# Optimization experiments

Hardware: AMD Instinct MI355X
Metric: run time of the kernel (lower is better)

Reference implementation:

```python
import jax, jax.numpy as jnp
import numpy as np

DIM_IN = 1024
DIM_OUT = 1024
NUM_HEADS = 16
HEAD_DIM = DIM_OUT // NUM_HEADS


def setup_inputs() -> dict:
    key = jax.random.key(0)
    k1, k2, k3, k4 = jax.random.split(key, 4)
    X = jax.random.normal(k1, (4, 2048, DIM_IN), dtype=jnp.float32)
    W_qkv = jax.random.normal(k2, (DIM_IN, 3 * DIM_OUT), dtype=jnp.float32) * (DIM_IN ** -0.5)
    W_out = jax.random.normal(k3, (DIM_OUT, DIM_OUT), dtype=jnp.float32) * (DIM_OUT ** -0.5)
    b_out = jax.random.normal(k4, (DIM_OUT,), dtype=jnp.float32) * 0.01
    return {"X": X, "W_qkv": W_qkv, "W_out": W_out, "b_out": b_out}


def reference(X, W_qkv, W_out, b_out):
    B, S, _ = X.shape
    qkv = X @ W_qkv  # [B, S, 3*dim_out]
    qkv = qkv.reshape(B, S, 3, NUM_HEADS, HEAD_DIM).transpose(2, 0, 3, 1, 4)
    q, k, v = qkv[0], qkv[1], qkv[2]  # each [B, H, S, hd]
    scores = jnp.einsum('bhqd,bhkd->bhqk', q, k)  # [B, H, S, S]
    causal = jnp.triu(jnp.ones((S, S), dtype=bool), k=1)
    scores = jnp.where(causal, -jnp.inf, scores)
    attn = jax.nn.softmax(scores * (HEAD_DIM ** -0.5), axis=-1)
    ctx = jnp.einsum('bhqk,bhkd->bhqd', attn, v)  # [B, H, S, hd]
    ctx = ctx.transpose(0, 2, 1, 3).reshape(B, S, DIM_OUT)
    return ctx @ W_out + b_out
```

## Files before the change

kernel.cpp:

```cpp
#include <hip/hip_runtime.h>
#include <hip/hip_bf16.h>

typedef __bf16 bf16_t;
typedef __bf16 bf16x8 __attribute__((ext_vector_type(8)));
typedef __bf16 bf16x4 __attribute__((ext_vector_type(4)));
typedef float f32x4 __attribute__((ext_vector_type(4)));
typedef float f32x16 __attribute__((ext_vector_type(16)));
typedef unsigned int u32x4 __attribute__((ext_vector_type(4)));

#define AS1(p) ((const __attribute__((address_space(1))) void*)(p))
#define AS3(p) ((__attribute__((address_space(3))) void*)(p))

#define QSCALE 0.1803368801111204f

__global__ void cast_x_kernel(const float* __restrict__ X, bf16_t* __restrict__ Xb) {
  int i = (blockIdx.x * 256 + threadIdx.x) * 4;
  float4 v = *(const float4*)(X + i);
  bf16x4 o;
  o[0] = (bf16_t)v.x; o[1] = (bf16_t)v.y; o[2] = (bf16_t)v.z; o[3] = (bf16_t)v.w;
  *(bf16x4*)(Xb + i) = o;
}

__global__ void transpose_cast_kernel(const float* __restrict__ W, bf16_t* __restrict__ Wt,
                                      int K, int N) {
  __shared__ float tile[32][33];
  int n0 = blockIdx.x * 32, k0 = blockIdx.y * 32;
  int tx = threadIdx.x, ty = threadIdx.y;
  for (int r = ty; r < 32; r += 8)
    tile[r][tx] = W[(size_t)(k0 + r) * N + n0 + tx];
  __syncthreads();
  for (int r = ty; r < 32; r += 8)
    Wt[(size_t)(n0 + r) * K + k0 + tx] = (bf16_t)tile[tx][r];
}

__global__ __launch_bounds__(256) void gemm_qkv_kernel(
    const bf16_t* __restrict__ A, const bf16_t* __restrict__ Bt,
    bf16_t* __restrict__ Qb, bf16_t* __restrict__ Kb, bf16_t* __restrict__ Vt) {
  __shared__ __align__(16) bf16_t As[128 * 32];
  __shared__ __align__(16) bf16_t Bs[128 * 32];
  const int tid = threadIdx.x;
  const int lane = tid & 63, wave = tid >> 6;
  const int quad = lane >> 4, l15 = lane & 15;
  const int wr = wave >> 1, wc = wave & 1;
  const int m0 = blockIdx.x * 128, n0 = blockIdx.y * 128;
  f32x4 acc[4][4];
  const f32x4 vzero = {0.f, 0.f, 0.f, 0.f};
#pragma unroll
  for (int i = 0; i < 4; i++)
#pragma unroll
    for (int j = 0; j < 4; j++) acc[i][j] = vzero;

  for (int kb = 0; kb < 1024; kb += 32) {
    __syncthreads();
#pragma unroll
    for (int i = 0; i < 2; i++) {
      int c = i * 256 + tid;
      int row = c >> 2, kc = c & 3;
      __builtin_amdgcn_global_load_lds(AS1(A + (size_t)(m0 + row) * 1024 + kb + kc * 8),
                                       AS3(As + c * 8), 16, 0, 0);
    }
#pragma unroll
    for (int i = 0; i < 2; i++) {
      int c = i * 256 + tid;
      int row = c >> 2, kc = c & 3;
      __builtin_amdgcn_global_load_lds(AS1(Bt + (size_t)(n0 + row) * 1024 + kb + kc * 8),
                                       AS3(Bs + c * 8), 16, 0, 0);
    }
    __builtin_amdgcn_s_waitcnt(0);
    __syncthreads();
    bf16x8 af[4], bfr[4];
#pragma unroll
    for (int t = 0; t < 4; t++) {
      af[t]  = *(const bf16x8*)(As + (wr * 64 + t * 16 + l15) * 32 + quad * 8);
      bfr[t] = *(const bf16x8*)(Bs + (wc * 64 + t * 16 + l15) * 32 + quad * 8);
    }
#pragma unroll
    for (int mt = 0; mt < 4; mt++)
#pragma unroll
      for (int nt = 0; nt < 4; nt++)
        acc[mt][nt] = __builtin_amdgcn_mfma_f32_16x16x32_bf16(af[mt], bfr[nt], acc[mt][nt], 0, 0, 0);
  }
#pragma unroll
  for (int nt = 0; nt < 4; nt++) {
    int gn = n0 + wc * 64 + nt * 16 + l15;
    int which = gn >> 10;
    int rem = gn & 1023;
    int hh = rem >> 6, dd = rem & 63;
    if (which == 2) {
#pragma unroll
      for (int mt = 0; mt < 4; mt++) {
        int gm0 = m0 + wr * 64 + mt * 16 + quad * 4;
        int b = gm0 >> 11, s = gm0 & 2047;
        bf16x4 o;
#pragma unroll
        for (int r = 0; r < 4; r++) o[r] = (bf16_t)acc[mt][nt][r];
        *(bf16x4*)(Vt + ((size_t)((b << 4) + hh) * 64 + dd) * 2048 + s) = o;
      }
    } else {
      bf16_t* dst = (which == 0) ? Qb : Kb;
      float scl = (which == 0) ? QSCALE : 1.0f;
#pragma unroll
      for (int mt = 0; mt < 4; mt++) {
#pragma unroll
        for (int r = 0; r < 4; r++) {
          int gm = m0 + wr * 64 + mt * 16 + quad * 4 + r;
          int b = gm >> 11, s = gm & 2047;
          dst[((size_t)((b << 4) + hh) * 2048 + s) * 64 + dd] = (bf16_t)(acc[mt][nt][r] * scl);
        }
      }
    }
  }
}

__device__ inline unsigned pack_bf16x2(float a, float b) {
  unsigned short lo = __builtin_bit_cast(unsigned short, (bf16_t)a);
  unsigned short hi = __builtin_bit_cast(unsigned short, (bf16_t)b);
  return (unsigned)lo | ((unsigned)hi << 16);
}

__global__ __launch_bounds__(256, 4) void attn_kernel(
    const bf16_t* __restrict__ Qg_, const bf16_t* __restrict__ Kg_,
    const bf16_t* __restrict__ Vtg_, bf16_t* __restrict__ ctx) {
  __shared__ __align__(16) bf16_t Ksm[2][64 * 64];
  __shared__ __align__(16) bf16_t Vsm[2][64 * 64];
  const int tid = threadIdx.x;
  const int lane = tid & 63, w = tid >> 6;
  const int l31 = lane & 31, hl = lane >> 5;
  const int krow = (l31 & 0x13) | ((l31 & 4) << 1) | ((l31 & 8) >> 1);

  const int bh = blockIdx.x & 63;
  const int g = blockIdx.x >> 6;
  const int gr = g >> 2, gc = g & 3;
  const int qb = (gr == 0) ? (15 - gc) : (gr == 1) ? (8 + gc) : (gr == 2) ? (7 - gc) : gc;
  const int b = bh >> 4, h = bh & 15;
  const size_t base = (size_t)bh * 2048 * 64;
  const bf16_t* Qg = Qg_ + base;
  const bf16_t* Kg = Kg_ + base;
  const bf16_t* Vtg = Vtg_ + base;

  int kadr[4];
#pragma unroll
  for (int kk = 0; kk < 4; kk++)
    kadr[kk] = (krow * 8 + ((kk * 2 + hl) ^ (krow & 7))) * 8;
  int vadr[2];
#pragma unroll
  for (int nv = 0; nv < 2; nv++) {
    const int dr = nv * 32 + l31;
    vadr[nv] = (dr * 8 + (hl ^ (dr & 7))) * 8;
  }

  auto stage_kv = [&](int bb, int jn) {
#pragma unroll
    for (int i = 0; i < 2; i++) {
      int slot = i * 256 + tid;
      int row = slot >> 3, c = (slot & 7) ^ (row & 7);
      __builtin_amdgcn_global_load_lds(AS1(Kg + ((size_t)jn * 64 + row) * 64 + c * 8),
                                       AS3(&Ksm[bb][0] + slot * 8), 16, 0, 0);
    }
#pragma unroll
    for (int i = 0; i < 2; i++) {
      int slot = i * 256 + tid;
      int d = slot >> 3, c = (slot & 7) ^ (d & 7);
      __builtin_amdgcn_global_load_lds(AS1(Vtg + (size_t)d * 2048 + jn * 64 + c * 8),
                                       AS3(&Vsm[bb][0] + slot * 8), 16, 0, 0);
    }
  };

  bf16x8 bone;
#pragma unroll
  for (int e = 0; e < 8; e++) bone[e] = (bf16_t)1.0f;
  f32x16 zc;
#pragma unroll
  for (int e = 0; e < 16; e++) zc[e] = 0.f;

  const int J = 2 * (qb + 1);
  const int qrel = qb * 128 + w * 32;
  const int qg = qrel + l31;

  bf16x8 aq[4];
#pragma unroll
  for (int kk = 0; kk < 4; kk++)
    aq[kk] = *(const bf16x8*)(Qg + (size_t)qg * 64 + kk * 16 + hl * 8);

  f32x16 Oacc[2], Lacc;
#pragma unroll
  for (int e = 0; e < 16; e++) { Oacc[0][e] = 0.f; Oacc[1][e] = 0.f; Lacc[e] = 0.f; }

  int cur = 0;
  stage_kv(0, 0);

  for (int j = 0; j < J; j++) {
    asm volatile("s_waitcnt vmcnt(0)" ::: "memory");
    __syncthreads();
    if (j + 1 < J) stage_kv(cur ^ 1, j + 1);

    const bf16_t* Kb = &Ksm[cur][0];
    const bf16_t* Vb = &Vsm[cur][0];
    const int k0 = j * 64;

    auto nt_body = [&](int nt, bool masked) {
      __builtin_amdgcn_s_setprio(1);
      bf16x8 ak = *(const bf16x8*)(Kb + nt * 2048 + kadr[0]);
      f32x16 sc = __builtin_amdgcn_mfma_f32_32x32x16_bf16(ak, aq[0], zc, 0, 0, 0);
#pragma unroll
      for (int kk = 1; kk < 4; kk++) {
        ak = *(const bf16x8*)(Kb + nt * 2048 + kadr[kk]);
        sc = __builtin_amdgcn_mfma_f32_32x32x16_bf16(ak, aq[kk], sc, 0, 0, 0);
      }
      __builtin_amdgcn_s_setprio(0);

      float p[16];
#pragma unroll
      for (int r = 0; r < 16; r++) {
        const int koff = hl * 8 + (r & 7) + 16 * (r >> 3);
        p[r] = (masked && (koff > l31)) ? 0.f : __builtin_exp2f(sc[r]);
      }

      u32x4 w0, w1;
      w0[0] = pack_bf16x2(p[0], p[1]);   w0[1] = pack_bf16x2(p[2], p[3]);
      w0[2] = pack_bf16x2(p[4], p[5]);   w0[3] = pack_bf16x2(p[6], p[7]);
      w1[0] = pack_bf16x2(p[8], p[9]);   w1[1] = pack_bf16x2(p[10], p[11]);
      w1[2] = pack_bf16x2(p[12], p[13]); w1[3] = pack_bf16x2(p[14], p[15]);
      bf16x8 pa0 = __builtin_bit_cast(bf16x8, w0);
      bf16x8 pa1 = __builtin_bit_cast(bf16x8, w1);

      __builtin_amdgcn_s_setprio(1);
      Lacc = __builtin_amdgcn_mfma_f32_32x32x16_bf16(pa0, bone, Lacc, 0, 0, 0);
      Lacc = __builtin_amdgcn_mfma_f32_32x32x16_bf16(pa1, bone, Lacc, 0, 0, 0);
#pragma unroll
      for (int nv = 0; nv < 2; nv++) {
        bf16x8 bv0 = *(const bf16x8*)(Vb + (vadr[nv] ^ ((nt * 4 + 0) * 8)));
        Oacc[nv] = __builtin_amdgcn_mfma_f32_32x32x16_bf16(pa0, bv0, Oacc[nv], 0, 0, 0);
        bf16x8 bv1 = *(const bf16x8*)(Vb + (vadr[nv] ^ ((nt * 4 + 2) * 8)));
        Oacc[nv] = __builtin_amdgcn_mfma_f32_32x32x16_bf16(pa1, bv1, Oacc[nv], 0, 0, 0);
      }
      __builtin_amdgcn_s_setprio(0);
    };

#pragma unroll
    for (int nt = 0; nt < 2; nt++) {
      const int kk0 = k0 + nt * 32;
      if (kk0 <= qrel) nt_body(nt, kk0 == qrel);
    }
    cur ^= 1;
  }

#pragma unroll
  for (int r = 0; r < 16; r++) {
    const int crow = (r & 3) + 8 * (r >> 2) + 4 * hl;
    const float rl = __builtin_amdgcn_rcpf(Lacc[r]);
    const int qrow = qb * 128 + w * 32 + crow;
#pragma unroll
    for (int nv = 0; nv < 2; nv++)
      ctx[((size_t)b * 2048 + qrow) * 1024 + h * 64 + nv * 32 + l31] =
          (bf16_t)(Oacc[nv][r] * rl);
  }
}

__global__ __launch_bounds__(256) void gemm_out_kernel(
    const bf16_t* __restrict__ A, const bf16_t* __restrict__ Bt,
    const float* __restrict__ bias, float* __restrict__ out) {
  __shared__ __align__(16) bf16_t As[128 * 32];
  __shared__ __align__(16) bf16_t Bs[128 * 32];
  const int tid = threadIdx.x;
  const int lane = tid & 63, wave = tid >> 6;
  const int quad = lane >> 4, l15 = lane & 15;
  const int wr = wave >> 1, wc = wave & 1;
  const int m0 = blockIdx.x * 128, n0 = blockIdx.y * 128;
  f32x4 acc[4][4];
  const f32x4 vzero = {0.f, 0.f, 0.f, 0.f};
#pragma unroll
  for (int i = 0; i < 4; i++)
#pragma unroll
    for (int j = 0; j < 4; j++) acc[i][j] = vzero;

  for (int kb = 0; kb < 1024; kb += 32) {
    __syncthreads();
#pragma unroll
    for (int i = 0; i < 2; i++) {
      int c = i * 256 + tid;
      int row = c >> 2, kc = c & 3;
      __builtin_amdgcn_global_load_lds(AS1(A + (size_t)(m0 + row) * 1024 + kb + kc * 8),
                                       AS3(As + c * 8), 16, 0, 0);
    }
#pragma unroll
    for (int i = 0; i < 2; i++) {
      int c = i * 256 + tid;
      int row = c >> 2, kc = c & 3;
      __builtin_amdgcn_global_load_lds(AS1(Bt + (size_t)(n0 + row) * 1024 + kb + kc * 8),
                                       AS3(Bs + c * 8), 16, 0, 0);
    }
    __builtin_amdgcn_s_waitcnt(0);
    __syncthreads();
    bf16x8 af[4], bfr[4];
#pragma unroll
    for (int t = 0; t < 4; t++) {
      af[t]  = *(const bf16x8*)(As + (wr * 64 + t * 16 + l15) * 32 + quad * 8);
      bfr[t] = *(const bf16x8*)(Bs + (wc * 64 + t * 16 + l15) * 32 + quad * 8);
    }
#pragma unroll
    for (int mt = 0; mt < 4; mt++)
#pragma unroll
      for (int nt = 0; nt < 4; nt++)
        acc[mt][nt] = __builtin_amdgcn_mfma_f32_16x16x32_bf16(af[mt], bfr[nt], acc[mt][nt], 0, 0, 0);
  }
#pragma unroll
  for (int nt = 0; nt < 4; nt++) {
    int gn = n0 + wc * 64 + nt * 16 + l15;
    float bv = bias[gn];
#pragma unroll
    for (int mt = 0; mt < 4; mt++) {
#pragma unroll
      for (int r = 0; r < 4; r++) {
        int gm = m0 + wr * 64 + mt * 16 + quad * 4 + r;
        out[(size_t)gm * 1024 + gn] = acc[mt][nt][r] + bv;
      }
    }
  }
}

extern "C" void kernel_launch(void* const* d_in, const int* in_sizes, int n_in,
                              void* d_out, int out_size, void* d_ws, size_t ws_size,
                              hipStream_t stream) {
  (void)in_sizes; (void)n_in; (void)out_size; (void)ws_size;
  const float* X     = (const float*)d_in[0];
  const float* W_qkv = (const float*)d_in[1];
  const float* W_out = (const float*)d_in[2];
  const float* b_out = (const float*)d_in[3];
  float* out = (float*)d_out;

  char* ws = (char*)d_ws;
  bf16_t* Xb    = (bf16_t*)(ws);
  bf16_t* Wqkvt = (bf16_t*)(ws + 16777216);
  bf16_t* Woutt = (bf16_t*)(ws + 23068672);
  bf16_t* Qb    = (bf16_t*)(ws + 25165824);
  bf16_t* Kb    = (bf16_t*)(ws + 41943040);
  bf16_t* Vt    = (bf16_t*)(ws + 58720256);
  bf16_t* ctx   = (bf16_t*)(ws + 75497472);

  cast_x_kernel<<<8192, 256, 0, stream>>>(X, Xb);
  transpose_cast_kernel<<<dim3(96, 32), dim3(32, 8), 0, stream>>>(W_qkv, Wqkvt, 1024, 3072);
  transpose_cast_kernel<<<dim3(32, 32), dim3(32, 8), 0, stream>>>(W_out, Woutt, 1024, 1024);
  gemm_qkv_kernel<<<dim3(64, 24), 256, 0, stream>>>(Xb, Wqkvt, Qb, Kb, Vt);
  attn_kernel<<<dim3(1024), 256, 0, stream>>>(Qb, Kb, Vt, ctx);
  gemm_out_kernel<<<dim3(64, 8), 256, 0, stream>>>(ctx, Woutt, b_out, out);
}
```

Baseline: 252.2 us.

## Double-buffer GEMM LDS staging and compute softmax row sums on VALU

Both GEMM kernels now keep two LDS buffers, so the next K-slice is prefetched while MFMAs run on the current one. This removes the full load-then-compute stall on every iteration. In attention, the row-sum MFMAs against a ones vector are replaced by per-lane scalar adds plus a cross-half shuffle and an LDS exchange. The QK^T MFMA chain is also split into two independent accumulators to shorten the dependency chain. The costs are doubled LDS use in the GEMMs, extra VALU adds, and a shared-memory round trip at the end of attention.

```diff
diff --git a/kernel.cpp b/kernel.cpp
--- a/kernel.cpp
+++ b/kernel.cpp
@@ -36,8 +36,8 @@
 __global__ __launch_bounds__(256) void gemm_qkv_kernel(
     const bf16_t* __restrict__ A, const bf16_t* __restrict__ Bt,
     bf16_t* __restrict__ Qb, bf16_t* __restrict__ Kb, bf16_t* __restrict__ Vt) {
-  __shared__ __align__(16) bf16_t As[128 * 32];
-  __shared__ __align__(16) bf16_t Bs[128 * 32];
+  __shared__ __align__(16) bf16_t As[2][128 * 32];
+  __shared__ __align__(16) bf16_t Bs[2][128 * 32];
   const int tid = threadIdx.x;
   const int lane = tid & 63, wave = tid >> 6;
   const int quad = lane >> 4, l15 = lane & 15;
@@ -50,35 +50,41 @@
 #pragma unroll
     for (int j = 0; j < 4; j++) acc[i][j] = vzero;
 
-  for (int kb = 0; kb < 1024; kb += 32) {
-    __syncthreads();
+  auto stage = [&](int bb, int kb) {
 #pragma unroll
     for (int i = 0; i < 2; i++) {
       int c = i * 256 + tid;
       int row = c >> 2, kc = c & 3;
       __builtin_amdgcn_global_load_lds(AS1(A + (size_t)(m0 + row) * 1024 + kb + kc * 8),
-                                       AS3(As + c * 8), 16, 0, 0);
+                                       AS3(&As[bb][0] + c * 8), 16, 0, 0);
     }
 #pragma unroll
     for (int i = 0; i < 2; i++) {
       int c = i * 256 + tid;
       int row = c >> 2, kc = c & 3;
       __builtin_amdgcn_global_load_lds(AS1(Bt + (size_t)(n0 + row) * 1024 + kb + kc * 8),
-                                       AS3(Bs + c * 8), 16, 0, 0);
-    }
-    __builtin_amdgcn_s_waitcnt(0);
+                                       AS3(&Bs[bb][0] + c * 8), 16, 0, 0);
+    }
+  };
+
+  stage(0, 0);
+  int cur = 0;
+  for (int kb = 0; kb < 1024; kb += 32) {
+    asm volatile("s_waitcnt vmcnt(0)" ::: "memory");
     __syncthreads();
+    if (kb + 32 < 1024) stage(cur ^ 1, kb + 32);
     bf16x8 af[4], bfr[4];
 #pragma unroll
     for (int t = 0; t < 4; t++) {
-      af[t]  = *(const bf16x8*)(As + (wr * 64 + t * 16 + l15) * 32 + quad * 8);
-      bfr[t] = *(const bf16x8*)(Bs + (wc * 64 + t * 16 + l15) * 32 + quad * 8);
+      af[t]  = *(const bf16x8*)(&As[cur][0] + (wr * 64 + t * 16 + l15) * 32 + quad * 8);
+      bfr[t] = *(const bf16x8*)(&Bs[cur][0] + (wc * 64 + t * 16 + l15) * 32 + quad * 8);
     }
 #pragma unroll
     for (int mt = 0; mt < 4; mt++)
 #pragma unroll
       for (int nt = 0; nt < 4; nt++)
         acc[mt][nt] = __builtin_amdgcn_mfma_f32_16x16x32_bf16(af[mt], bfr[nt], acc[mt][nt], 0, 0, 0);
+    cur ^= 1;
   }
 #pragma unroll
   for (int nt = 0; nt < 4; nt++) {
@@ -123,6 +129,7 @@
     const bf16_t* __restrict__ Vtg_, bf16_t* __restrict__ ctx) {
   __shared__ __align__(16) bf16_t Ksm[2][64 * 64];
   __shared__ __align__(16) bf16_t Vsm[2][64 * 64];
+  __shared__ float Lsh[128];
   const int tid = threadIdx.x;
   const int lane = tid & 63, w = tid >> 6;
   const int l31 = lane & 31, hl = lane >> 5;
@@ -166,9 +173,6 @@
     }
   };
 
-  bf16x8 bone;
-#pragma unroll
-  for (int e = 0; e < 8; e++) bone[e] = (bf16_t)1.0f;
   f32x16 zc;
 #pragma unroll
   for (int e = 0; e < 16; e++) zc[e] = 0.f;
@@ -182,9 +186,10 @@
   for (int kk = 0; kk < 4; kk++)
     aq[kk] = *(const bf16x8*)(Qg + (size_t)qg * 64 + kk * 16 + hl * 8);
 
-  f32x16 Oacc[2], Lacc;
-#pragma unroll
-  for (int e = 0; e < 16; e++) { Oacc[0][e] = 0.f; Oacc[1][e] = 0.f; Lacc[e] = 0.f; }
+  f32x16 Oacc[2];
+#pragma unroll
+  for (int e = 0; e < 16; e++) { Oacc[0][e] = 0.f; Oacc[1][e] = 0.f; }
+  float Lpart = 0.f;
 
   int cur = 0;
   stage_kv(0, 0);
@@ -200,20 +205,28 @@
 
     auto nt_body = [&](int nt, bool masked) {
       __builtin_amdgcn_s_setprio(1);
-      bf16x8 ak = *(const bf16x8*)(Kb + nt * 2048 + kadr[0]);
-      f32x16 sc = __builtin_amdgcn_mfma_f32_32x32x16_bf16(ak, aq[0], zc, 0, 0, 0);
-#pragma unroll
-      for (int kk = 1; kk < 4; kk++) {
-        ak = *(const bf16x8*)(Kb + nt * 2048 + kadr[kk]);
-        sc = __builtin_amdgcn_mfma_f32_32x32x16_bf16(ak, aq[kk], sc, 0, 0, 0);
-      }
+      bf16x8 a0 = *(const bf16x8*)(Kb + nt * 2048 + kadr[0]);
+      bf16x8 a1 = *(const bf16x8*)(Kb + nt * 2048 + kadr[1]);
+      f32x16 sa = __builtin_amdgcn_mfma_f32_32x32x16_bf16(a0, aq[0], zc, 0, 0, 0);
+      f32x16 sb = __builtin_amdgcn_mfma_f32_32x32x16_bf16(a1, aq[1], zc, 0, 0, 0);
+      bf16x8 a2 = *(const bf16x8*)(Kb + nt * 2048 + kadr[2]);
+      bf16x8 a3 = *(const bf16x8*)(Kb + nt * 2048 + kadr[3]);
+      sa = __builtin_amdgcn_mfma_f32_32x32x16_bf16(a2, aq[2], sa, 0, 0, 0);
+      sb = __builtin_amdgcn_mfma_f32_32x32x16_bf16(a3, aq[3], sb, 0, 0, 0);
       __builtin_amdgcn_s_setprio(0);
 
       float p[16];
 #pragma unroll
       for (int r = 0; r < 16; r++) {
         const int koff = hl * 8 + (r & 7) + 16 * (r >> 3);
-        p[r] = (masked && (koff > l31)) ? 0.f : __builtin_exp2f(sc[r]);
+        const float x = sa[r] + sb[r];
+        p[r] = (masked && (koff > l31)) ? 0.f : __builtin_exp2f(x);
+      }
+
+      {
+        float a0s = p[0] + p[1], a1s = p[2] + p[3], a2s = p[4] + p[5], a3s = p[6] + p[7];
+        float a4s = p[8] + p[9], a5s = p[10] + p[11], a6s = p[12] + p[13], a7s = p[14] + p[15];
+        Lpart += ((a0s + a1s) + (a2s + a3s)) + ((a4s + a5s) + (a6s + a7s));
       }
 
       u32x4 w0, w1;
@@ -225,8 +238,6 @@
       bf16x8 pa1 = __builtin_bit_cast(bf16x8, w1);
 
       __builtin_amdgcn_s_setprio(1);
-      Lacc = __builtin_amdgcn_mfma_f32_32x32x16_bf16(pa0, bone, Lacc, 0, 0, 0);
-      Lacc = __builtin_amdgcn_mfma_f32_32x32x16_bf16(pa1, bone, Lacc, 0, 0, 0);
 #pragma unroll
       for (int nv = 0; nv < 2; nv++) {
         bf16x8 bv0 = *(const bf16x8*)(Vb + (vadr[nv] ^ ((nt * 4 + 0) * 8)));
@@ -245,10 +256,13 @@
     cur ^= 1;
   }
 
+  float Lf = Lpart + __shfl_xor(Lpart, 32, 64);
+  if (hl == 0) Lsh[w * 32 + l31] = Lf;
+  asm volatile("s_waitcnt lgkmcnt(0)" ::: "memory");
 #pragma unroll
   for (int r = 0; r < 16; r++) {
     const int crow = (r & 3) + 8 * (r >> 2) + 4 * hl;
-    const float rl = __builtin_amdgcn_rcpf(Lacc[r]);
+    const float rl = __builtin_amdgcn_rcpf(Lsh[w * 32 + crow]);
     const int qrow = qb * 128 + w * 32 + crow;
 #pragma unroll
     for (int nv = 0; nv < 2; nv++)
@@ -260,8 +274,8 @@
 __global__ __launch_bounds__(256) void gemm_out_kernel(
     const bf16_t* __restrict__ A, const bf16_t* __restrict__ Bt,
     const float* __restrict__ bias, float* __restrict__ out) {
-  __shared__ __align__(16) bf16_t As[128 * 32];
-  __shared__ __align__(16) bf16_t Bs[128 * 32];
+  __shared__ __align__(16) bf16_t As[2][128 * 32];
+  __shared__ __align__(16) bf16_t Bs[2][128 * 32];
   const int tid = threadIdx.x;
   const int lane = tid & 63, wave = tid >> 6;
   const int quad = lane >> 4, l15 = lane & 15;
@@ -274,35 +288,41 @@
 #pragma unroll
     for (int j = 0; j < 4; j++) acc[i][j] = vzero;
 
-  for (int kb = 0; kb < 1024; kb += 32) {
-    __syncthreads();
+  auto stage = [&](int bb, int kb) {
 #pragma unroll
     for (int i = 0; i < 2; i++) {
       int c = i * 256 + tid;
       int row = c >> 2, kc = c & 3;
       __builtin_amdgcn_global_load_lds(AS1(A + (size_t)(m0 + row) * 1024 + kb + kc * 8),
-                                       AS3(As + c * 8), 16, 0, 0);
+                                       AS3(&As[bb][0] + c * 8), 16, 0, 0);
     }
 #pragma unroll
     for (int i = 0; i < 2; i++) {
       int c = i * 256 + tid;
       int row = c >> 2, kc = c & 3;
       __builtin_amdgcn_global_load_lds(AS1(Bt + (size_t)(n0 + row) * 1024 + kb + kc * 8),
-                                       AS3(Bs + c * 8), 16, 0, 0);
-    }
-    __builtin_amdgcn_s_waitcnt(0);
+                                       AS3(&Bs[bb][0] + c * 8), 16, 0, 0);
+    }
+  };
+
+  stage(0, 0);
+  int cur = 0;
+  for (int kb = 0; kb < 1024; kb += 32) {
+    asm volatile("s_waitcnt vmcnt(0)" ::: "memory");
     __syncthreads();
+    if (kb + 32 < 1024) stage(cur ^ 1, kb + 32);
     bf16x8 af[4], bfr[4];
 #pragma unroll
     for (int t = 0; t < 4; t++) {
-      af[t]  = *(const bf16x8*)(As + (wr * 64 + t * 16 + l15) * 32 + quad * 8);
-      bfr[t] = *(const bf16x8*)(Bs + (wc * 64 + t * 16 + l15) * 32 + quad * 8);
+      af[t]  = *(const bf16x8*)(&As[cur][0] + (wr * 64 + t * 16 + l15) * 32 + quad * 8);
+      bfr[t] = *(const bf16x8*)(&Bs[cur][0] + (wc * 64 + t * 16 + l15) * 32 + quad * 8);
     }
 #pragma unroll
     for (int mt = 0; mt < 4; mt++)
 #pragma unroll
       for (int nt = 0; nt < 4; nt++)
         acc[mt][nt] = __builtin_amdgcn_mfma_f32_16x16x32_bf16(af[mt], bfr[nt], acc[mt][nt], 0, 0, 0);
+    cur ^= 1;
   }
 #pragma unroll
   for (int nt = 0; nt < 4; nt++) {
```

Measured after the change: 260.6 us. 1.03x slower.

## Fuse prep kernels, split QK accumulation chain, compute softmax denominator on VALU

Applied to the files above, without the earlier changes.

The X cast and both weight transpose-casts now run in a single prep launch that dispatches on block index, removing two kernel launches. In attention, the QK^T dot product is split into two independent MFMA accumulators and summed afterwards, which shortens the dependent MFMA chain. The row-sum MFMAs against a ones vector are replaced by per-lane VALU additions of the fp32 probabilities, a cross-half shuffle, and an LDS lookup that remaps rows to the output layout. This drops two MFMAs per tile at the cost of extra adds and one extra zero-initialized accumulator, and the denominator now sums unrounded fp32 values rather than bf16-rounded ones.

```diff
diff --git a/kernel.cpp b/kernel.cpp
--- a/kernel.cpp
+++ b/kernel.cpp
@@ -13,19 +13,27 @@
 
 #define QSCALE 0.1803368801111204f
 
-__global__ void cast_x_kernel(const float* __restrict__ X, bf16_t* __restrict__ Xb) {
-  int i = (blockIdx.x * 256 + threadIdx.x) * 4;
-  float4 v = *(const float4*)(X + i);
-  bf16x4 o;
-  o[0] = (bf16_t)v.x; o[1] = (bf16_t)v.y; o[2] = (bf16_t)v.z; o[3] = (bf16_t)v.w;
-  *(bf16x4*)(Xb + i) = o;
-}
-
-__global__ void transpose_cast_kernel(const float* __restrict__ W, bf16_t* __restrict__ Wt,
-                                      int K, int N) {
+__global__ __launch_bounds__(256) void prep_kernel(
+    const float* __restrict__ X, bf16_t* __restrict__ Xb,
+    const float* __restrict__ Wqkv, bf16_t* __restrict__ Wqkvt,
+    const float* __restrict__ Wout, bf16_t* __restrict__ Woutt) {
   __shared__ float tile[32][33];
-  int n0 = blockIdx.x * 32, k0 = blockIdx.y * 32;
-  int tx = threadIdx.x, ty = threadIdx.y;
+  int bid = blockIdx.x;
+  if (bid < 8192) {
+    int i = (bid * 256 + threadIdx.x) * 4;
+    float4 v = *(const float4*)(X + i);
+    bf16x4 o;
+    o[0] = (bf16_t)v.x; o[1] = (bf16_t)v.y; o[2] = (bf16_t)v.z; o[3] = (bf16_t)v.w;
+    *(bf16x4*)(Xb + i) = o;
+    return;
+  }
+  bid -= 8192;
+  const float* W; bf16_t* Wt; int N, bx, by;
+  if (bid < 3072) { W = Wqkv; Wt = Wqkvt; N = 3072; bx = bid % 96; by = bid / 96; }
+  else { bid -= 3072; W = Wout; Wt = Woutt; N = 1024; bx = bid & 31; by = bid >> 5; }
+  const int K = 1024;
+  int tx = threadIdx.x & 31, ty = threadIdx.x >> 5;
+  int n0 = bx * 32, k0 = by * 32;
   for (int r = ty; r < 32; r += 8)
     tile[r][tx] = W[(size_t)(k0 + r) * N + n0 + tx];
   __syncthreads();
@@ -123,6 +131,7 @@
     const bf16_t* __restrict__ Vtg_, bf16_t* __restrict__ ctx) {
   __shared__ __align__(16) bf16_t Ksm[2][64 * 64];
   __shared__ __align__(16) bf16_t Vsm[2][64 * 64];
+  __shared__ float Lsh[128];
   const int tid = threadIdx.x;
   const int lane = tid & 63, w = tid >> 6;
   const int l31 = lane & 31, hl = lane >> 5;
@@ -166,9 +175,6 @@
     }
   };
 
-  bf16x8 bone;
-#pragma unroll
-  for (int e = 0; e < 8; e++) bone[e] = (bf16_t)1.0f;
   f32x16 zc;
 #pragma unroll
   for (int e = 0; e < 16; e++) zc[e] = 0.f;
@@ -182,9 +188,10 @@
   for (int kk = 0; kk < 4; kk++)
     aq[kk] = *(const bf16x8*)(Qg + (size_t)qg * 64 + kk * 16 + hl * 8);
 
-  f32x16 Oacc[2], Lacc;
-#pragma unroll
-  for (int e = 0; e < 16; e++) { Oacc[0][e] = 0.f; Oacc[1][e] = 0.f; Lacc[e] = 0.f; }
+  f32x16 Oacc[2];
+#pragma unroll
+  for (int e = 0; e < 16; e++) { Oacc[0][e] = 0.f; Oacc[1][e] = 0.f; }
+  float Lpart = 0.f;
 
   int cur = 0;
   stage_kv(0, 0);
@@ -200,20 +207,28 @@
 
     auto nt_body = [&](int nt, bool masked) {
       __builtin_amdgcn_s_setprio(1);
-      bf16x8 ak = *(const bf16x8*)(Kb + nt * 2048 + kadr[0]);
-      f32x16 sc = __builtin_amdgcn_mfma_f32_32x32x16_bf16(ak, aq[0], zc, 0, 0, 0);
-#pragma unroll
-      for (int kk = 1; kk < 4; kk++) {
-        ak = *(const bf16x8*)(Kb + nt * 2048 + kadr[kk]);
-        sc = __builtin_amdgcn_mfma_f32_32x32x16_bf16(ak, aq[kk], sc, 0, 0, 0);
-      }
+      bf16x8 a0 = *(const bf16x8*)(Kb + nt * 2048 + kadr[0]);
+      bf16x8 a1 = *(const bf16x8*)(Kb + nt * 2048 + kadr[1]);
+      f32x16 sa = __builtin_amdgcn_mfma_f32_32x32x16_bf16(a0, aq[0], zc, 0, 0, 0);
+      f32x16 sb = __builtin_amdgcn_mfma_f32_32x32x16_bf16(a1, aq[1], zc, 0, 0, 0);
+      bf16x8 a2 = *(const bf16x8*)(Kb + nt * 2048 + kadr[2]);
+      bf16x8 a3 = *(const bf16x8*)(Kb + nt * 2048 + kadr[3]);
+      sa = __builtin_amdgcn_mfma_f32_32x32x16_bf16(a2, aq[2], sa, 0, 0, 0);
+      sb = __builtin_amdgcn_mfma_f32_32x32x16_bf16(a3, aq[3], sb, 0, 0, 0);
       __builtin_amdgcn_s_setprio(0);
 
       float p[16];
 #pragma unroll
       for (int r = 0; r < 16; r++) {
         const int koff = hl * 8 + (r & 7) + 16 * (r >> 3);
-        p[r] = (masked && (koff > l31)) ? 0.f : __builtin_exp2f(sc[r]);
+        const float x = sa[r] + sb[r];
+        p[r] = (masked && (koff > l31)) ? 0.f : __builtin_exp2f(x);
+      }
+
+      {
+        float a0s = p[0] + p[1], a1s = p[2] + p[3], a2s = p[4] + p[5], a3s = p[6] + p[7];
+        float a4s = p[8] + p[9], a5s = p[10] + p[11], a6s = p[12] + p[13], a7s = p[14] + p[15];
+        Lpart += ((a0s + a1s) + (a2s + a3s)) + ((a4s + a5s) + (a6s + a7s));
       }
 
       u32x4 w0, w1;
@@ -225,8 +240,6 @@
       bf16x8 pa1 = __builtin_bit_cast(bf16x8, w1);
 
       __builtin_amdgcn_s_setprio(1);
-      Lacc = __builtin_amdgcn_mfma_f32_32x32x16_bf16(pa0, bone, Lacc, 0, 0, 0);
-      Lacc = __builtin_amdgcn_mfma_f32_32x32x16_bf16(pa1, bone, Lacc, 0, 0, 0);
 #pragma unroll
       for (int nv = 0; nv < 2; nv++) {
         bf16x8 bv0 = *(const bf16x8*)(Vb + (vadr[nv] ^ ((nt * 4 + 0) * 8)));
@@ -245,10 +258,13 @@
     cur ^= 1;
   }
 
+  float Lf = Lpart + __shfl_xor(Lpart, 32, 64);
+  if (hl == 0) Lsh[w * 32 + l31] = Lf;
+  asm volatile("s_waitcnt lgkmcnt(0)" ::: "memory");
 #pragma unroll
   for (int r = 0; r < 16; r++) {
     const int crow = (r & 3) + 8 * (r >> 2) + 4 * hl;
-    const float rl = __builtin_amdgcn_rcpf(Lacc[r]);
+    const float rl = __builtin_amdgcn_rcpf(Lsh[w * 32 + crow]);
     const int qrow = qb * 128 + w * 32 + crow;
 #pragma unroll
     for (int nv = 0; nv < 2; nv++)
@@ -338,9 +354,7 @@
   bf16_t* Vt    = (bf16_t*)(ws + 58720256);
   bf16_t* ctx   = (bf16_t*)(ws + 75497472);
 
-  cast_x_kernel<<<8192, 256, 0, stream>>>(X, Xb);
-  transpose_cast_kernel<<<dim3(96, 32), dim3(32, 8), 0, stream>>>(W_qkv, Wqkvt, 1024, 3072);
-  transpose_cast_kernel<<<dim3(32, 32), dim3(32, 8), 0, stream>>>(W_out, Woutt, 1024, 1024);
+  prep_kernel<<<12288, 256, 0, stream>>>(X, Xb, W_qkv, Wqkvt, W_out, Woutt);
   gemm_qkv_kernel<<<dim3(64, 24), 256, 0, stream>>>(Xb, Wqkvt, Qb, Kb, Vt);
   attn_kernel<<<dim3(1024), 256, 0, stream>>>(Qb, Kb, Vt, ctx);
   gemm_out_kernel<<<dim3(64, 8), 256, 0, stream>>>(ctx, Woutt, b_out, out);
```

New measurement: 247.3 us. 2.0% less time.
